# Kernel tuning notes

Measured on AMD Instinct MI355X. Metric: run time of the kernel, lower is better.

## Reference

```python
import jax, jax.numpy as jnp
import numpy as np

N_STATE = 128      # HiPPO state size (hardcoded N=128 in module)
SEQ = 8192         # sequence length
D_HEAD = 16        # d_model=128 // n_head=8, used only for score scaling
OUT_DIM = 1000     # hardcoded self.out_dim
STEP = 1e-3        # step_size


def _legs_matrices(N):
    # HiPPO-LegS: A[n,k] = -sqrt(2n+1)sqrt(2k+1) (n>k), -(n+1) (n==k), 0 else; B[n]=sqrt(2n+1)
    n = np.arange(N, dtype=np.float64)
    pre = np.sqrt(2.0 * n + 1.0)
    A = -np.tril(pre[:, None] * pre[None, :], -1) - np.diag(n + 1.0)
    B = pre.copy()
    return A, B


def setup_inputs() -> dict:
    key = jax.random.key(0)
    kq, kk, kv, kw = jax.random.split(key, 4)
    A_np, B_np = _legs_matrices(N_STATE)
    A = jnp.asarray(A_np, jnp.float32)
    B = jnp.asarray(B_np, jnp.float32)
    # ZOH discretization (GBT_alpha=2.0 > 1 in repo => zero-order hold)
    GA = jax.scipy.linalg.expm(STEP * A)                       # (N, N)
    GB = jnp.linalg.solve(A, (GA - jnp.eye(N_STATE)) @ B)      # (N,)
    # xavier-uniform proj kernel (128 -> 1000), zero bias
    lim = float(np.sqrt(6.0 / (N_STATE + OUT_DIM)))
    Wp = jax.random.uniform(kw, (N_STATE, OUT_DIM), jnp.float32, -lim, lim)
    bp = jnp.zeros((OUT_DIM,), jnp.float32)
    return {
        "query": jax.random.normal(kq, (SEQ, 1), jnp.float32),
        "key": jax.random.normal(kk, (SEQ, 1), jnp.float32),
        "value": jax.random.normal(kv, (SEQ, 1), jnp.float32),
        "GA": GA,
        "GB": GB,
        "Wp": Wp,
        "bp": bp,
    }


def _hippo_scan(GA, GB, fs):
    # fs: (3, S) scalar input sequences; carry c: (3, N)
    def step(c, ft):
        c = c @ GA.T + ft[:, None] * GB[None, :]
        return c, c
    c0 = jnp.zeros((fs.shape[0], GA.shape[0]), GA.dtype)
    _, cs = jax.lax.scan(step, c0, fs.T)   # cs: (S, 3, N)
    return cs


def reference(query, key, value, GA, GB, Wp, bp):
    fs = jnp.stack([query[:, 0], key[:, 0], value[:, 0]])  # (3, S)
    cs = _hippo_scan(GA, GB, fs)                            # (S, 3, N)
    q, k, v = cs[:, 0, :], cs[:, 1, :], cs[:, 2, :]         # (S, N) each
    score = (q @ k.T) / jnp.sqrt(jnp.asarray(D_HEAD, q.dtype))  # (S, S)
    attn = jax.nn.softmax(score, axis=-1)
    context = attn @ v                                      # (S, N)
    out = context @ Wp + bp                                 # (S, OUT_DIM)
    return out, attn
```

## Files before the change

kernel.cpp:

```cpp
#include <hip/hip_runtime.h>

static constexpr int N  = 128;
static constexpr int S  = 8192;
static constexpr int L  = 128;
static constexpr int NC = 64;
static constexpr int OD = 1000;
static constexpr int KSPLIT = 16;
#define SCL 0.25f

typedef unsigned short u16;
typedef __attribute__((ext_vector_type(4))) unsigned short us4;
typedef __attribute__((ext_vector_type(8))) unsigned short us8;
typedef __attribute__((ext_vector_type(8))) short bf16x8;
typedef __attribute__((ext_vector_type(4))) float f32x4;

__device__ __forceinline__ u16 f2bf(float x){
  unsigned u = __float_as_uint(x);
  u += 0x7FFFu + ((u >> 16) & 1u);
  return (u16)(u >> 16);
}
__device__ __forceinline__ float bf2f(u16 h){
  return __uint_as_float(((unsigned)h) << 16);
}


__global__ void k_copyT(const float* __restrict__ GA, float* __restrict__ QT1){
  int idx = blockIdx.x*256 + threadIdx.x;
  int m = idx >> 7, n = idx & 127;
  QT1[idx] = GA[n*N + m];
}

__global__ __launch_bounds__(256) void k_powmm(float* QT, int mlev){
  int i = blockIdx.z + 1;
  const float* Am = QT + (size_t)mlev*(N*N);
  const float* Ai = QT + (size_t)i*(N*N);
  float* C = QT + (size_t)(mlev+i)*(N*N);
  __shared__ __align__(16) float As[16][68];
  __shared__ __align__(16) float Bs[16][68];
  int bm = blockIdx.y, bn = blockIdx.x;
  int tx = threadIdx.x, ty = threadIdx.y;
  int tid = ty*16 + tx;
  float acc[4][4] = {};
  for (int kt = 0; kt < N; kt += 16){
    int row = tid >> 2, kc = (tid & 3) << 2;
    float4 av = *(const float4*)(Am + (size_t)(bm*64+row)*N + kt + kc);
    As[kc+0][row]=av.x; As[kc+1][row]=av.y; As[kc+2][row]=av.z; As[kc+3][row]=av.w;
    int bk = tid >> 4, c0 = (tid & 15) << 2;
    *(float4*)&Bs[bk][c0] = *(const float4*)(Ai + (size_t)(kt+bk)*N + bn*64 + c0);
    __syncthreads();
#pragma unroll
    for (int kk = 0; kk < 16; ++kk){
      float4 a = *(const float4*)&As[kk][ty*4];
      float4 b = *(const float4*)&Bs[kk][tx*4];
      float aa[4]={a.x,a.y,a.z,a.w}, bb[4]={b.x,b.y,b.z,b.w};
#pragma unroll
      for (int ii=0; ii<4; ++ii)
#pragma unroll
        for (int jj=0; jj<4; ++jj) acc[ii][jj] += aa[ii]*bb[jj];
    }
    __syncthreads();
  }
#pragma unroll
  for (int ii=0; ii<4; ++ii){
    float4 vst = make_float4(acc[ii][0],acc[ii][1],acc[ii][2],acc[ii][3]);
    *(float4*)(C + (size_t)(bm*64+ty*4+ii)*N + bn*64 + tx*4) = vst;
  }
}

__global__ void k_g(const float* __restrict__ QT, const float* __restrict__ GB,
                    float* __restrict__ g){
  int kb = blockIdx.x;
  int n = threadIdx.x;
  if (kb == 0){ g[n] = GB[n]; return; }
  const float* Qk = QT + (size_t)kb*(N*N);
  float acc = 0.0f;
  for (int m = 0; m < N; ++m) acc += Qk[m*N + n]*GB[m];
  g[kb*N + n] = acc;
}

__global__ __launch_bounds__(256) void k_fill_local(const float* __restrict__ fq,
                             const float* __restrict__ fk, const float* __restrict__ fv,
                             const float* __restrict__ g, float* __restrict__ cs){
  int tile = blockIdx.x;
  int s = blockIdx.y, j = blockIdx.z;
  const float* f = (s==0)? fq : (s==1)? fk : fv;
  __shared__ float flp[256];
  __shared__ __align__(16) float Bs[16][68];
  int tx = threadIdx.x, ty = threadIdx.y;
  int tid = ty*16 + tx;
  flp[tid] = (tid < 128) ? 0.0f : f[j*L + tid - 128];
  int ti = tile >> 1, tj = tile & 1;
  float acc[4][4] = {};
  int kmax = (ti == 0) ? 64 : 128;
  for (int kt = 0; kt < kmax; kt += 16){
    int bk = tid >> 4, c0 = (tid & 15) << 2;
    *(float4*)&Bs[bk][c0] = *(const float4*)(g + (size_t)(kt+bk)*N + tj*64 + c0);
    __syncthreads();
#pragma unroll
    for (int kk = 0; kk < 16; ++kk){
      float4 b = *(const float4*)&Bs[kk][tx*4];
      int base = 128 + ti*64 + ty*4 - kt - kk;
      float aa[4] = {flp[base], flp[base+1], flp[base+2], flp[base+3]};
      float bb[4] = {b.x, b.y, b.z, b.w};
#pragma unroll
      for (int ii=0; ii<4; ++ii)
#pragma unroll
        for (int jj=0; jj<4; ++jj) acc[ii][jj] += aa[ii]*bb[jj];
    }
    __syncthreads();
  }
#pragma unroll
  for (int ii=0; ii<4; ++ii){
    int row = ti*64 + ty*4 + ii;
    float4 vst = make_float4(acc[ii][0],acc[ii][1],acc[ii][2],acc[ii][3]);
    *(float4*)(cs + ((size_t)s*S + (size_t)j*L + row)*N + tj*64 + tx*4) = vst;
  }
}

__global__ void k_bscan(const float* __restrict__ QT, const float* __restrict__ cs,
                        float* __restrict__ bounds){
  __shared__ float bc[3][N];
  __shared__ float bnx[3][N];
  int tid = threadIdx.x;
  int s = tid >> 7, n = tid & 127;
  const float* QL = QT + (size_t)L*(N*N);
  bc[s][n] = 0.0f;
  bounds[(0*3+s)*N + n] = 0.0f;
  __syncthreads();
  for (int j = 0; j < NC; ++j){
    float acc = cs[((size_t)s*S + (size_t)j*L + 127)*N + n];
    for (int m = 0; m < N; ++m) acc += QL[m*N+n]*bc[s][m];
    bnx[s][n] = acc;
    bounds[((j+1)*3+s)*N + n] = acc;
    __syncthreads();
    bc[s][n] = bnx[s][n];
    __syncthreads();
  }
}

__global__ __launch_bounds__(256) void k_fill_bound(const float* __restrict__ QT,
                          const float* __restrict__ bounds, float* __restrict__ cs){
  int i = blockIdx.x;
  int jg = blockIdx.y;
  __shared__ float Qs[N*N];
  int tid = threadIdx.x;
  int p = tid >> 7, n = tid & 127;
  const float* Qg = QT + (size_t)(i+1)*(N*N);
  for (int idx = tid; idx < N*N; idx += 256) Qs[idx] = Qg[idx];
  __syncthreads();
  for (int r = 0; r < 24; ++r){
    int task = jg*48 + p*24 + r;
    int j = task/3, s = task - 3*j;
    const float* b = bounds + (size_t)task*N;
    float a0=0.f, a1=0.f, a2=0.f, a3=0.f;
    for (int m = 0; m < N; m += 4){
      a0 += Qs[(m+0)*N+n]*b[m+0];
      a1 += Qs[(m+1)*N+n]*b[m+1];
      a2 += Qs[(m+2)*N+n]*b[m+2];
      a3 += Qs[(m+3)*N+n]*b[m+3];
    }
    cs[((size_t)s*S + (size_t)j*L + i)*N + n] += (a0+a1)+(a2+a3);
  }
}

__global__ void k_split_qk(const float* __restrict__ cs,
                           u16* __restrict__ sh, u16* __restrict__ sl){
  size_t i = ((size_t)blockIdx.x*256 + threadIdx.x) << 2;
  float4 v = *(const float4*)(cs + i);
  us4 h, l;
  h[0]=f2bf(v.x); l[0]=f2bf(v.x - bf2f(h[0]));
  h[1]=f2bf(v.y); l[1]=f2bf(v.y - bf2f(h[1]));
  h[2]=f2bf(v.z); l[2]=f2bf(v.z - bf2f(h[2]));
  h[3]=f2bf(v.w); l[3]=f2bf(v.w - bf2f(h[3]));
  *(us4*)(sh + i) = h;
  *(us4*)(sl + i) = l;
}

__global__ __launch_bounds__(256) void k_split_vT(const float* __restrict__ vs,
                           u16* __restrict__ vth, u16* __restrict__ vtl){
  __shared__ u16 Th[128*72];
  __shared__ u16 Tl[128*72];
  int t0 = blockIdx.x * 64;
  int tid = threadIdx.x;
  for (int c = tid; c < 2048; c += 256){
    int i = c >> 5, n0 = (c & 31) << 2;
    float4 v = *(const float4*)(vs + (size_t)(t0 + i)*N + n0);
    u16 h;
    h = f2bf(v.x); Th[(n0+0)*72 + i] = h; Tl[(n0+0)*72 + i] = f2bf(v.x - bf2f(h));
    h = f2bf(v.y); Th[(n0+1)*72 + i] = h; Tl[(n0+1)*72 + i] = f2bf(v.y - bf2f(h));
    h = f2bf(v.z); Th[(n0+2)*72 + i] = h; Tl[(n0+2)*72 + i] = f2bf(v.z - bf2f(h));
    h = f2bf(v.w); Th[(n0+3)*72 + i] = h; Tl[(n0+3)*72 + i] = f2bf(v.w - bf2f(h));
  }
  __syncthreads();
  for (int c = tid; c < 1024; c += 256){
    int n = c >> 3, tc = (c & 7) << 3;
    *(us8*)(vth + (size_t)n*S + t0 + tc) = *(const us8*)&Th[n*72 + tc];
    *(us8*)(vtl + (size_t)n*S + t0 + tc) = *(const us8*)&Tl[n*72 + tc];
  }
}

__global__ __launch_bounds__(256) void k_score_mfma(
    const u16* __restrict__ qh, const u16* __restrict__ ql,
    const u16* __restrict__ kh, const u16* __restrict__ kl,
    float* __restrict__ attn){
  __shared__ u16 Ah[128*40], Al[128*40], Bh[128*40], Bl[128*40];
  int bm = blockIdx.y, bn = blockIdx.x;
  int tid = threadIdx.x;
  int lane = tid & 63, w = tid >> 6;
  int wr = w >> 1, wc = w & 1;
  f32x4 acc[4][4] = {};
  int rA = wr*64 + (lane & 15);
  int rB = wc*64 + (lane & 15);
  int kg = (lane >> 4) << 3;
  for (int kt = 0; kt < N; kt += 32){
    for (int c = tid; c < 512; c += 256){
      int r = c >> 2, k8 = (c & 3) << 3;
      size_t ga = (size_t)(bm*128 + r)*N + kt + k8;
      size_t gb = (size_t)(bn*128 + r)*N + kt + k8;
      int lo = r*40 + k8;
      *(us8*)&Ah[lo] = *(const us8*)(qh + ga);
      *(us8*)&Al[lo] = *(const us8*)(ql + ga);
      *(us8*)&Bh[lo] = *(const us8*)(kh + gb);
      *(us8*)&Bl[lo] = *(const us8*)(kl + gb);
    }
    __syncthreads();
    bf16x8 ah[4], al[4], bh[4], bl[4];
#pragma unroll
    for (int mi = 0; mi < 4; ++mi){
      ah[mi] = *(const bf16x8*)&Ah[(rA + mi*16)*40 + kg];
      al[mi] = *(const bf16x8*)&Al[(rA + mi*16)*40 + kg];
    }
#pragma unroll
    for (int ni = 0; ni < 4; ++ni){
      bh[ni] = *(const bf16x8*)&Bh[(rB + ni*16)*40 + kg];
      bl[ni] = *(const bf16x8*)&Bl[(rB + ni*16)*40 + kg];
    }
#pragma unroll
    for (int mi = 0; mi < 4; ++mi)
#pragma unroll
      for (int ni = 0; ni < 4; ++ni){
        acc[mi][ni] = __builtin_amdgcn_mfma_f32_16x16x32_bf16(ah[mi], bh[ni], acc[mi][ni], 0,0,0);
        acc[mi][ni] = __builtin_amdgcn_mfma_f32_16x16x32_bf16(ah[mi], bl[ni], acc[mi][ni], 0,0,0);
        acc[mi][ni] = __builtin_amdgcn_mfma_f32_16x16x32_bf16(al[mi], bh[ni], acc[mi][ni], 0,0,0);
      }
    __syncthreads();
  }
  int r0 = bm*128 + wr*64 + ((lane >> 4) << 2);
  int c0 = bn*128 + wc*64 + (lane & 15);
#pragma unroll
  for (int mi = 0; mi < 4; ++mi)
#pragma unroll
    for (int ni = 0; ni < 4; ++ni)
#pragma unroll
      for (int r = 0; r < 4; ++r)
        attn[(size_t)(r0 + mi*16 + r)*S + c0 + ni*16] = acc[mi][ni][r] * SCL;
}

__global__ __launch_bounds__(256) void k_softmax(float* __restrict__ attn){
  __shared__ __align__(16) float rowb[S];
  __shared__ float red[256];
  int t = blockIdx.x;
  int tid = threadIdx.x;
  float4* g4 = (float4*)(attn + (size_t)t*S);
  float4* r4 = (float4*)rowb;
  float mx = -3.0e38f;
  for (int u = tid; u < S/4; u += 256){
    float4 v = g4[u];
    r4[u] = v;
    mx = fmaxf(mx, fmaxf(fmaxf(v.x,v.y), fmaxf(v.z,v.w)));
  }
  red[tid] = mx; __syncthreads();
  for (int st = 128; st > 0; st >>= 1){
    if (tid < st) red[tid] = fmaxf(red[tid], red[tid+st]);
    __syncthreads();
  }
  mx = red[0];
  __syncthreads();
  float sum = 0.0f;
  for (int u = tid; u < S/4; u += 256){
    float4 v = r4[u];
    v.x = __expf(v.x - mx); v.y = __expf(v.y - mx);
    v.z = __expf(v.z - mx); v.w = __expf(v.w - mx);
    r4[u] = v;
    sum += v.x + v.y + v.z + v.w;
  }
  red[tid] = sum; __syncthreads();
  for (int st = 128; st > 0; st >>= 1){
    if (tid < st) red[tid] += red[tid+st];
    __syncthreads();
  }
  float inv = 1.0f / red[0];
  for (int u = tid; u < S/4; u += 256){
    float4 v = r4[u];
    v.x *= inv; v.y *= inv; v.z *= inv; v.w *= inv;
    g4[u] = v;
  }
}

__global__ __launch_bounds__(256) void k_context_mfma(const float* __restrict__ attn,
                       const u16* __restrict__ vth, const u16* __restrict__ vtl,
                       float* __restrict__ dst, int mode){
  __shared__ u16 Ah[128*40], Al[128*40], Bh[128*40], Bl[128*40];
  int kz = blockIdx.x, bm = blockIdx.y;
  int tid = threadIdx.x;
  int lane = tid & 63, w = tid >> 6;
  int wr = w >> 1, wc = w & 1;
  const int KC = S / KSPLIT;
  int k0 = kz*KC;
  f32x4 acc[4][4] = {};
  int rA = wr*64 + (lane & 15);
  int rB = wc*64 + (lane & 15);
  int kg = (lane >> 4) << 3;
  for (int kt = 0; kt < KC; kt += 32){
    for (int c = tid; c < 1024; c += 256){
      int r = c >> 3, c4 = (c & 7) << 2;
      float4 v = *(const float4*)(attn + (size_t)(bm*128 + r)*S + k0 + kt + c4);
      us4 h, l;
      h[0]=f2bf(v.x); l[0]=f2bf(v.x - bf2f(h[0]));
      h[1]=f2bf(v.y); l[1]=f2bf(v.y - bf2f(h[1]));
      h[2]=f2bf(v.z); l[2]=f2bf(v.z - bf2f(h[2]));
      h[3]=f2bf(v.w); l[3]=f2bf(v.w - bf2f(h[3]));
      int lo = r*40 + c4;
      *(us4*)&Ah[lo] = h;
      *(us4*)&Al[lo] = l;
    }
    for (int c = tid; c < 512; c += 256){
      int n = c >> 2, k8 = (c & 3) << 3;
      size_t gb = (size_t)n*S + k0 + kt + k8;
      int lo = n*40 + k8;
      *(us8*)&Bh[lo] = *(const us8*)(vth + gb);
      *(us8*)&Bl[lo] = *(const us8*)(vtl + gb);
    }
    __syncthreads();
    bf16x8 ah[4], al[4], bh[4], bl[4];
#pragma unroll
    for (int mi = 0; mi < 4; ++mi){
      ah[mi] = *(const bf16x8*)&Ah[(rA + mi*16)*40 + kg];
      al[mi] = *(const bf16x8*)&Al[(rA + mi*16)*40 + kg];
    }
#pragma unroll
    for (int ni = 0; ni < 4; ++ni){
      bh[ni] = *(const bf16x8*)&Bh[(rB + ni*16)*40 + kg];
      bl[ni] = *(const bf16x8*)&Bl[(rB + ni*16)*40 + kg];
    }
#pragma unroll
    for (int mi = 0; mi < 4; ++mi)
#pragma unroll
      for (int ni = 0; ni < 4; ++ni){
        acc[mi][ni] = __builtin_amdgcn_mfma_f32_16x16x32_bf16(ah[mi], bh[ni], acc[mi][ni], 0,0,0);
        acc[mi][ni] = __builtin_amdgcn_mfma_f32_16x16x32_bf16(ah[mi], bl[ni], acc[mi][ni], 0,0,0);
        acc[mi][ni] = __builtin_amdgcn_mfma_f32_16x16x32_bf16(al[mi], bh[ni], acc[mi][ni], 0,0,0);
      }
    __syncthreads();
  }
  int r0 = bm*128 + wr*64 + ((lane >> 4) << 2);
  int c0 = wc*64 + (lane & 15);
  if (mode == 0){
    float* P = dst + (size_t)kz*S*N;
#pragma unroll
    for (int mi = 0; mi < 4; ++mi)
#pragma unroll
      for (int ni = 0; ni < 4; ++ni)
#pragma unroll
        for (int r = 0; r < 4; ++r)
          P[(size_t)(r0 + mi*16 + r)*N + c0 + ni*16] = acc[mi][ni][r];
  } else {
#pragma unroll
    for (int mi = 0; mi < 4; ++mi)
#pragma unroll
      for (int ni = 0; ni < 4; ++ni)
#pragma unroll
        for (int r = 0; r < 4; ++r)
          atomicAdd(&dst[(size_t)(r0 + mi*16 + r)*N + c0 + ni*16], acc[mi][ni][r]);
  }
}

__global__ __launch_bounds__(256) void k_reduce(const float* __restrict__ part,
                                                float* __restrict__ ctx){
  size_t idx = (size_t)blockIdx.x*256 + threadIdx.x;
  const float4* p4 = (const float4*)part;
  float4 acc = p4[idx];
  const size_t stride = (size_t)S*N/4;
#pragma unroll
  for (int kz = 1; kz < KSPLIT; ++kz){
    float4 v = p4[(size_t)kz*stride + idx];
    acc.x += v.x; acc.y += v.y; acc.z += v.z; acc.w += v.w;
  }
  ((float4*)ctx)[idx] = acc;
}

__global__ __launch_bounds__(256) void k_out(const float* __restrict__ ctx,
                   const float* __restrict__ Wp, const float* __restrict__ bp,
                   float* __restrict__ out){
  __shared__ __align__(16) float As[16][68];
  __shared__ __align__(16) float Bs[16][68];
  int bn = blockIdx.x;
  int bm = blockIdx.y;
  int tx = threadIdx.x, ty = threadIdx.y;
  int tid = ty*16 + tx;
  float acc[4][4] = {};
  for (int kt = 0; kt < N; kt += 16){
    int row = tid >> 2, kc = (tid & 3) << 2;
    float4 av = *(const float4*)(ctx + (size_t)(bm*64+row)*N + kt + kc);
    As[kc+0][row]=av.x; As[kc+1][row]=av.y; As[kc+2][row]=av.z; As[kc+3][row]=av.w;
    int bk = tid >> 4, c0 = (tid & 15) << 2;
#pragma unroll
    for (int jj = 0; jj < 4; ++jj){
      int c = bn*64 + c0 + jj;
      Bs[bk][c0+jj] = (c < OD) ? Wp[(size_t)(kt+bk)*OD + c] : 0.0f;
    }
    __syncthreads();
#pragma unroll
    for (int kk = 0; kk < 16; ++kk){
      float4 a = *(const float4*)&As[kk][ty*4];
      float4 b = *(const float4*)&Bs[kk][tx*4];
      float aa[4]={a.x,a.y,a.z,a.w}, bb[4]={b.x,b.y,b.z,b.w};
#pragma unroll
      for (int ii=0; ii<4; ++ii)
#pragma unroll
        for (int jj=0; jj<4; ++jj) acc[ii][jj] += aa[ii]*bb[jj];
    }
    __syncthreads();
  }
#pragma unroll
  for (int ii=0; ii<4; ++ii){
    int r = bm*64 + ty*4 + ii;
#pragma unroll
    for (int jj=0; jj<4; ++jj){
      int c = bn*64 + tx*4 + jj;
      if (c < OD) out[(size_t)r*OD + c] = acc[ii][jj] + bp[c];
    }
  }
}

extern "C" void kernel_launch(void* const* d_in, const int* in_sizes, int n_in,
                              void* d_out, int out_size, void* d_ws, size_t ws_size,
                              hipStream_t stream){
  const float* fq = (const float*)d_in[0];
  const float* fk = (const float*)d_in[1];
  const float* fv = (const float*)d_in[2];
  const float* GA = (const float*)d_in[3];
  const float* GB = (const float*)d_in[4];
  const float* Wp = (const float*)d_in[5];
  const float* bp = (const float*)d_in[6];
  float* out  = (float*)d_out;
  float* attn = out + (size_t)S*OD;

  float* ws     = (float*)d_ws;
  float* QT     = ws;
  float* g      = QT + (size_t)129*N*N;
  float* bounds = g + (size_t)L*N;
  float* cs     = bounds + (size_t)(NC+1)*3*N;
  float* ctx    = cs + (size_t)3*S*N;
  u16*   qkh    = (u16*)(ctx + (size_t)S*N);
  u16*   qkl    = qkh + (size_t)2*S*N;
  u16*   vth    = qkl + (size_t)2*S*N;
  u16*   vtl    = vth + (size_t)S*N;
  float* part   = (float*)(vtl + (size_t)S*N);
  size_t need_part = ((size_t)(part - ws) + (size_t)KSPLIT*S*N) * sizeof(float);
  bool use_part = (ws_size >= need_part);

  k_copyT<<<64, 256, 0, stream>>>(GA, QT + (size_t)N*N);
  for (int m = 1; m < L; m <<= 1)
    k_powmm<<<dim3(2,2,m), dim3(16,16), 0, stream>>>(QT, m);
  k_g<<<128, 128, 0, stream>>>(QT, GB, g);
  k_fill_local<<<dim3(4,3,NC), dim3(16,16), 0, stream>>>(fq, fk, fv, g, cs);
  k_bscan<<<1, 384, 0, stream>>>(QT, cs, bounds);
  k_fill_bound<<<dim3(L,4), 256, 0, stream>>>(QT, bounds, cs);

  k_split_qk<<<(2*S*N)/1024, 256, 0, stream>>>(cs, qkh, qkl);
  k_split_vT<<<S/64, 256, 0, stream>>>(cs + (size_t)2*S*N, vth, vtl);

  k_score_mfma<<<dim3(S/128, S/128), 256, 0, stream>>>(
      qkh, qkl, qkh + (size_t)S*N, qkl + (size_t)S*N, attn);
  k_softmax<<<S, 256, 0, stream>>>(attn);
  if (use_part){
    k_context_mfma<<<dim3(KSPLIT, S/128), 256, 0, stream>>>(attn, vth, vtl, part, 0);
    k_reduce<<<(S*N/4)/256, 256, 0, stream>>>(part, ctx);
  } else {
    hipMemsetAsync(ctx, 0, (size_t)S*N*sizeof(float), stream);
    k_context_mfma<<<dim3(KSPLIT, S/128), 256, 0, stream>>>(attn, vth, vtl, ctx, 1);
  }
  k_out<<<dim3(16, S/64), dim3(16,16), 0, stream>>>(ctx, Wp, bp, out);
}
```

Measured before the change: 863.2 us.

## Fuse softmax into score and context kernels via per-tile row statistics

The score kernel now stages each 128x128 tile through shared memory, which gives coalesced float4 stores, and it computes per-tile row max and sum-of-exp partials. A small kernel reduces those partials into a row max and inverse sum. The context kernel then applies exp and normalisation while loading attn and writes the normalised values back. This drops the separate softmax pass over the 256MB attention matrix, which saves a full read and write, at the cost of serial per-row statistics loops in the score epilogue. Separately, the fill_bound kernel now processes four bound vectors per pass so each Qs load is reused across them.

```diff
diff --git a/kernel.cpp b/kernel.cpp
--- a/kernel.cpp
+++ b/kernel.cpp
@@ -22,7 +22,6 @@
 __device__ __forceinline__ float bf2f(u16 h){
   return __uint_as_float(((unsigned)h) << 16);
 }
-
 
 __global__ void k_copyT(const float* __restrict__ GA, float* __restrict__ QT1){
   int idx = blockIdx.x*256 + threadIdx.x;
@@ -148,18 +147,25 @@
   const float* Qg = QT + (size_t)(i+1)*(N*N);
   for (int idx = tid; idx < N*N; idx += 256) Qs[idx] = Qg[idx];
   __syncthreads();
-  for (int r = 0; r < 24; ++r){
-    int task = jg*48 + p*24 + r;
-    int j = task/3, s = task - 3*j;
-    const float* b = bounds + (size_t)task*N;
+  for (int r4 = 0; r4 < 24; r4 += 4){
+    int task0 = jg*48 + p*24 + r4;
+    const float* b0 = bounds + (size_t)task0*N;
+    const float* b1 = b0 + N;
+    const float* b2 = b0 + 2*N;
+    const float* b3 = b0 + 3*N;
     float a0=0.f, a1=0.f, a2=0.f, a3=0.f;
-    for (int m = 0; m < N; m += 4){
-      a0 += Qs[(m+0)*N+n]*b[m+0];
-      a1 += Qs[(m+1)*N+n]*b[m+1];
-      a2 += Qs[(m+2)*N+n]*b[m+2];
-      a3 += Qs[(m+3)*N+n]*b[m+3];
-    }
-    cs[((size_t)s*S + (size_t)j*L + i)*N + n] += (a0+a1)+(a2+a3);
+#pragma unroll 4
+    for (int m = 0; m < N; ++m){
+      float q = Qs[m*N + n];
+      a0 += q*b0[m]; a1 += q*b1[m]; a2 += q*b2[m]; a3 += q*b3[m];
+    }
+    float av[4] = {a0, a1, a2, a3};
+#pragma unroll
+    for (int q4 = 0; q4 < 4; ++q4){
+      int task = task0 + q4;
+      int j = task/3, s2 = task - 3*j;
+      cs[((size_t)s2*S + (size_t)j*L + i)*N + n] += av[q4];
+    }
   }
 }
 
@@ -202,8 +208,13 @@
 __global__ __launch_bounds__(256) void k_score_mfma(
     const u16* __restrict__ qh, const u16* __restrict__ ql,
     const u16* __restrict__ kh, const u16* __restrict__ kl,
-    float* __restrict__ attn){
-  __shared__ u16 Ah[128*40], Al[128*40], Bh[128*40], Bl[128*40];
+    float* __restrict__ attn, float* __restrict__ pmax, float* __restrict__ psum){
+  __shared__ __align__(16) u16 smem[4*128*40];
+  __shared__ float stats[128][2][2];
+  u16* Ah = smem;
+  u16* Al = smem + 5120;
+  u16* Bh = smem + 10240;
+  u16* Bl = smem + 15360;
   int bm = blockIdx.y, bn = blockIdx.x;
   int tid = threadIdx.x;
   int lane = tid & 63, w = tid >> 6;
@@ -245,68 +256,70 @@
       }
     __syncthreads();
   }
-  int r0 = bm*128 + wr*64 + ((lane >> 4) << 2);
-  int c0 = bn*128 + wc*64 + (lane & 15);
-#pragma unroll
-  for (int mi = 0; mi < 4; ++mi)
-#pragma unroll
-    for (int ni = 0; ni < 4; ++ni)
-#pragma unroll
-      for (int r = 0; r < 4; ++r)
-        attn[(size_t)(r0 + mi*16 + r)*S + c0 + ni*16] = acc[mi][ni][r] * SCL;
-}
-
-__global__ __launch_bounds__(256) void k_softmax(float* __restrict__ attn){
-  __shared__ __align__(16) float rowb[S];
-  __shared__ float red[256];
-  int t = blockIdx.x;
-  int tid = threadIdx.x;
-  float4* g4 = (float4*)(attn + (size_t)t*S);
-  float4* r4 = (float4*)rowb;
-  float mx = -3.0e38f;
-  for (int u = tid; u < S/4; u += 256){
-    float4 v = g4[u];
-    r4[u] = v;
-    mx = fmaxf(mx, fmaxf(fmaxf(v.x,v.y), fmaxf(v.z,v.w)));
-  }
-  red[tid] = mx; __syncthreads();
-  for (int st = 128; st > 0; st >>= 1){
-    if (tid < st) red[tid] = fmaxf(red[tid], red[tid+st]);
-    __syncthreads();
-  }
-  mx = red[0];
-  __syncthreads();
-  float sum = 0.0f;
-  for (int u = tid; u < S/4; u += 256){
-    float4 v = r4[u];
-    v.x = __expf(v.x - mx); v.y = __expf(v.y - mx);
-    v.z = __expf(v.z - mx); v.w = __expf(v.w - mx);
-    r4[u] = v;
-    sum += v.x + v.y + v.z + v.w;
-  }
-  red[tid] = sum; __syncthreads();
-  for (int st = 128; st > 0; st >>= 1){
-    if (tid < st) red[tid] += red[tid+st];
-    __syncthreads();
-  }
-  float inv = 1.0f / red[0];
-  for (int u = tid; u < S/4; u += 256){
-    float4 v = r4[u];
-    v.x *= inv; v.y *= inv; v.z *= inv; v.w *= inv;
-    g4[u] = v;
-  }
-}
-
-__global__ __launch_bounds__(256) void k_context_mfma(const float* __restrict__ attn,
+  float* bounce = (float*)smem;
+  int r0l = wr*64 + ((lane >> 4) << 2);
+  int c0l = lane & 15;
+#pragma unroll
+  for (int half = 0; half < 2; ++half){
+    if (wc == half){
+#pragma unroll
+      for (int mi = 0; mi < 4; ++mi)
+#pragma unroll
+        for (int ni = 0; ni < 4; ++ni)
+#pragma unroll
+          for (int r = 0; r < 4; ++r)
+            bounce[(r0l + mi*16 + r)*68 + ni*16 + c0l] = acc[mi][ni][r]*SCL;
+    }
+    __syncthreads();
+    for (int c = tid; c < 2048; c += 256){
+      int r = c >> 4, c4 = (c & 15) << 2;
+      *(float4*)(attn + (size_t)(bm*128 + r)*S + bn*128 + half*64 + c4) =
+          *(const float4*)&bounce[r*68 + c4];
+    }
+    if (tid < 128){
+      int row = tid;
+      float m = -3.0e38f;
+      for (int c = 0; c < 64; ++c) m = fmaxf(m, bounce[row*68 + c]);
+      float sm = 0.0f;
+      for (int c = 0; c < 64; ++c) sm += __expf(bounce[row*68 + c] - m);
+      stats[row][half][0] = m; stats[row][half][1] = sm;
+    }
+    __syncthreads();
+  }
+  if (tid < 128){
+    float m0 = stats[tid][0][0], m1 = stats[tid][1][0];
+    float m = fmaxf(m0, m1);
+    float Z = stats[tid][0][1]*__expf(m0 - m) + stats[tid][1][1]*__expf(m1 - m);
+    pmax[(size_t)bn*S + bm*128 + tid] = m;
+    psum[(size_t)bn*S + bm*128 + tid] = Z;
+  }
+}
+
+__global__ void k_rowstat(const float* __restrict__ pmax, const float* __restrict__ psum,
+                          float* __restrict__ rowm, float* __restrict__ rowinv){
+  int t = blockIdx.x*256 + threadIdx.x;
+  float m = -3.0e38f;
+  for (int b = 0; b < 64; ++b) m = fmaxf(m, pmax[(size_t)b*S + t]);
+  float Z = 0.0f;
+  for (int b = 0; b < 64; ++b) Z += psum[(size_t)b*S + t]*__expf(pmax[(size_t)b*S + t] - m);
+  rowm[t] = m;
+  rowinv[t] = 1.0f/Z;
+}
+
+__global__ __launch_bounds__(256) void k_context_mfma(float* __restrict__ attn,
+                       const float* __restrict__ rowm, const float* __restrict__ rowinv,
                        const u16* __restrict__ vth, const u16* __restrict__ vtl,
                        float* __restrict__ dst, int mode){
   __shared__ u16 Ah[128*40], Al[128*40], Bh[128*40], Bl[128*40];
+  __shared__ float rm[128], ri[128];
   int kz = blockIdx.x, bm = blockIdx.y;
   int tid = threadIdx.x;
   int lane = tid & 63, w = tid >> 6;
   int wr = w >> 1, wc = w & 1;
   const int KC = S / KSPLIT;
   int k0 = kz*KC;
+  if (tid < 128){ rm[tid] = rowm[bm*128 + tid]; ri[tid] = rowinv[bm*128 + tid]; }
+  __syncthreads();
   f32x4 acc[4][4] = {};
   int rA = wr*64 + (lane & 15);
   int rB = wc*64 + (lane & 15);
@@ -314,7 +327,12 @@
   for (int kt = 0; kt < KC; kt += 32){
     for (int c = tid; c < 1024; c += 256){
       int r = c >> 3, c4 = (c & 7) << 2;
-      float4 v = *(const float4*)(attn + (size_t)(bm*128 + r)*S + k0 + kt + c4);
+      size_t gaddr = (size_t)(bm*128 + r)*S + k0 + kt + c4;
+      float4 v = *(const float4*)(attn + gaddr);
+      float m = rm[r], z = ri[r];
+      v.x = __expf(v.x - m)*z; v.y = __expf(v.y - m)*z;
+      v.z = __expf(v.z - m)*z; v.w = __expf(v.w - m)*z;
+      *(float4*)(attn + gaddr) = v;
       us4 h, l;
       h[0]=f2bf(v.x); l[0]=f2bf(v.x - bf2f(h[0]));
       h[1]=f2bf(v.y); l[1]=f2bf(v.y - bf2f(h[1]));
@@ -456,7 +474,11 @@
   u16*   qkl    = qkh + (size_t)2*S*N;
   u16*   vth    = qkl + (size_t)2*S*N;
   u16*   vtl    = vth + (size_t)S*N;
-  float* part   = (float*)(vtl + (size_t)S*N);
+  float* pmax   = (float*)(vtl + (size_t)S*N);
+  float* psum   = pmax + (size_t)(S/128)*S;
+  float* rowm   = psum + (size_t)(S/128)*S;
+  float* rowinv = rowm + S;
+  float* part   = rowinv + S;
   size_t need_part = ((size_t)(part - ws) + (size_t)KSPLIT*S*N) * sizeof(float);
   bool use_part = (ws_size >= need_part);
 
@@ -472,14 +494,14 @@
   k_split_vT<<<S/64, 256, 0, stream>>>(cs + (size_t)2*S*N, vth, vtl);
 
   k_score_mfma<<<dim3(S/128, S/128), 256, 0, stream>>>(
-      qkh, qkl, qkh + (size_t)S*N, qkl + (size_t)S*N, attn);
-  k_softmax<<<S, 256, 0, stream>>>(attn);
+      qkh, qkl, qkh + (size_t)S*N, qkl + (size_t)S*N, attn, pmax, psum);
+  k_rowstat<<<S/256, 256, 0, stream>>>(pmax, psum, rowm, rowinv);
   if (use_part){
-    k_context_mfma<<<dim3(KSPLIT, S/128), 256, 0, stream>>>(attn, vth, vtl, part, 0);
+    k_context_mfma<<<dim3(KSPLIT, S/128), 256, 0, stream>>>(attn, rowm, rowinv, vth, vtl, part, 0);
     k_reduce<<<(S*N/4)/256, 256, 0, stream>>>(part, ctx);
   } else {
     hipMemsetAsync(ctx, 0, (size_t)S*N*sizeof(float), stream);
-    k_context_mfma<<<dim3(KSPLIT, S/128), 256, 0, stream>>>(attn, vth, vtl, ctx, 1);
+    k_context_mfma<<<dim3(KSPLIT, S/128), 256, 0, stream>>>(attn, rowm, rowinv, vth, vtl, ctx, 1);
   }
   k_out<<<dim3(16, S/64), dim3(16,16), 0, stream>>>(ctx, Wp, bp, out);
 }
```

Result: slower. 892.7 us (+3.4%).
